# Kernel optimization log

Measured on AMD Instinct MI355X. Metric: run time of the kernel, lower is better.

Reference implementation:

```python
import jax, jax.numpy as jnp
import numpy as np
from jax import lax

MASK_STEEP = 4.0
MASK_SHIFT = 0.5
RESIST_TH = 0.225
RESIST_STEEP = 50.0
MAX_DOSE = 1.02
MIN_DOSE = 0.98
KD = 35  # kernel_dim1 == kernel_dim2


def setup_inputs() -> dict:
    key = jax.random.key(0)
    ks = jax.random.split(key, 7)
    N, H, W, K = 2, 1024, 1024, 24
    return {
        "mask_tile": jax.random.uniform(ks[0], (N, 1, H, W), dtype=jnp.float32),
        "kernel_focus_r": jax.random.normal(ks[1], (K, KD, KD), dtype=jnp.float32) * 0.02,
        "kernel_focus_i": jax.random.normal(ks[2], (K, KD, KD), dtype=jnp.float32) * 0.02,
        "kernel_defocus_r": jax.random.normal(ks[3], (K, KD, KD), dtype=jnp.float32) * 0.02,
        "kernel_defocus_i": jax.random.normal(ks[4], (K, KD, KD), dtype=jnp.float32) * 0.02,
        "kernel_focus_scale": jax.random.uniform(ks[5], (K, 1, 1), dtype=jnp.float32),
        "kernel_defocus_scale": jax.random.uniform(ks[6], (K, 1, 1), dtype=jnp.float32),
    }


def _avepool3(x):
    # nn.AvgPool2d(kernel=3, stride=1, pad=1) with count_include_pad=True ==
    # conv with a 3x3 ones/9 kernel and zero padding.
    k = jnp.ones((1, 1, 3, 3), x.dtype) / 9.0
    return lax.conv_general_dilated(
        x, k, window_strides=(1, 1), padding=[(1, 1), (1, 1)],
        dimension_numbers=("NCHW", "OIHW", "NCHW"))


def _dose_branch(spec, dose, kernel, scale, h, w):
    # spec: [N,1,KD,KD] complex; kernel: [K,KD,KD] complex; scale: [K,1,1]
    x = (spec * dose) * kernel[None]                 # [N,K,KD,KD] (repeat_interleave via broadcast, C=1)
    x = jnp.fft.ifft2(x, s=(h, w))                   # zero-pad to full tile, [N,K,h,w] complex
    inten = (x.real * x.real + x.imag * x.imag) * scale[None]
    inten = jnp.sum(inten, axis=1, keepdims=True)    # [N,1,h,w]
    resist = jax.nn.sigmoid(RESIST_STEEP * (inten - RESIST_TH))
    return resist, inten


def reference(mask_tile, kernel_focus_r, kernel_focus_i, kernel_defocus_r,
              kernel_defocus_i, kernel_focus_scale, kernel_defocus_scale):
    n, _, h, w = mask_tile.shape
    off = h // 2 - KD // 2
    mask = _avepool3(mask_tile)
    mask = jax.nn.sigmoid(MASK_STEEP * (mask - MASK_SHIFT))
    mf = jnp.fft.fftshift(jnp.fft.fft2(mask), axes=(-2, -1))  # [N,1,h,w] complex64
    spec = mf[:, :, off:off + KD, off:off + KD]               # [N,1,KD,KD]
    kf = kernel_focus_r + 1j * kernel_focus_i
    kdf = kernel_defocus_r + 1j * kernel_defocus_i
    nominal, x_out = _dose_branch(spec, 1.0, kf, kernel_focus_scale, h, w)
    outer, x_out_max = _dose_branch(spec, MAX_DOSE, kf, kernel_focus_scale, h, w)
    inner, x_out_min = _dose_branch(spec, MIN_DOSE, kdf, kernel_defocus_scale, h, w)
    return (nominal, inner, outer, x_out, x_out_min, x_out_max)
```

## Files before the change

kernel.cpp:

```cpp
#include <hip/hip_runtime.h>
#include <math.h>

#define NBATCH 2
#define HH 1024
#define WW 1024
#define KKER 24
#define KDIM 35
#define NPIX (HH*WW)
#define KSQ (KDIM*KDIM)
#define NDA 69
#define NTAU 9
#define NFR 18

#define G_OFF    0
#define SPEC_OFF (G_OFF + NBATCH*HH*NFR*2)
#define VP_OFF   (SPEC_OFF + NBATCH*KSQ*2)
#define V_OFF    (VP_OFF + NBATCH*2*KKER*NDA*KDIM*2)

__device__ __forceinline__ float2 cmadd(float2 p, float2 w, float2 u) {
    return make_float2(fmaf(p.x, w.x, fmaf(-p.y, w.y, u.x)),
                       fmaf(p.x, w.y, fmaf( p.y, w.x, u.y)));
}
__device__ __forceinline__ float sigm(float v) {
    return 1.f / (1.f + expf(-v));
}

__global__ __launch_bounds__(320) void fwd_rows(const float* __restrict__ mt, float* __restrict__ ws) {
    __shared__ __align__(16) float vs[1024];
    __shared__ float row[1056];
    __shared__ float2 twl[1024];
    __shared__ float2 P[16 * NFR];
    int bid = blockIdx.x;
    int n = bid >> 10, y = bid & 1023;
    int t = threadIdx.x;
    const float* base = mt + (size_t)n * NPIX;
    if (t < 256) {
        float4 a = ((const float4*)(base + (size_t)y * WW))[t];
        if (y > 0)    { float4 b = ((const float4*)(base + (size_t)(y - 1) * WW))[t];
                        a.x += b.x; a.y += b.y; a.z += b.z; a.w += b.w; }
        if (y < 1023) { float4 b = ((const float4*)(base + (size_t)(y + 1) * WW))[t];
                        a.x += b.x; a.y += b.y; a.z += b.z; a.w += b.w; }
        ((float4*)vs)[t] = a;
    }
    for (int j = t; j < 1024; j += 320) {
        float s, c;
        sincospif(-2.0f * (float)j * (1.0f / 1024.0f), &s, &c);
        twl[j] = make_float2(c, s);
    }
    __syncthreads();
    for (int x = t; x < 1024; x += 320) {
        float s = vs[x];
        if (x > 0)    s += vs[x - 1];
        if (x < 1023) s += vs[x + 1];
        s *= (1.0f / 9.0f);
        row[x + (x >> 5)] = sigm(4.0f * (s - 0.5f));
    }
    __syncthreads();
    if (t < 16 * NFR) {
        int q = t / NFR, m = t - q * NFR;
        float2 cm = twl[m];
        float ar = 0.f, ai = 0.f;
        #pragma unroll
        for (int sc = 0; sc < 2; ++sc) {
            int xs = q * 64 + sc * 32;
            unsigned j0 = ((unsigned)(m * xs)) & 1023u;
            float2 wv = twl[j0];
            float wr = wv.x, wi = wv.y;
            int rb = xs + (xs >> 5);
            #pragma unroll
            for (int i = 0; i < 32; ++i) {
                float val = row[rb + i];
                ar = fmaf(val, wr, ar);
                ai = fmaf(val, wi, ai);
                float nwr = fmaf(wr, cm.x, -wi * cm.y);
                float nwi = fmaf(wr, cm.y,  wi * cm.x);
                wr = nwr; wi = nwi;
            }
        }
        P[t] = make_float2(ar, ai);
    }
    __syncthreads();
    if (t < NFR) {
        float gr = 0.f, gi = 0.f;
        #pragma unroll
        for (int q = 0; q < 16; ++q) {
            gr += P[q * NFR + t].x;
            gi += P[q * NFR + t].y;
        }
        float2* Gp = (float2*)(ws + G_OFF) + (size_t)(n * HH + y) * NFR + t;
        *Gp = make_float2(gr, gi);
    }
}

__global__ __launch_bounds__(320) void fwd_cols(float* __restrict__ ws) {
    __shared__ float2 twl[1024];
    __shared__ float2 P[16 * NFR];
    int bid = blockIdx.x;
    int n = bid / KDIM, a = bid - n * KDIM;
    int t = threadIdx.x;
    for (int j = t; j < 1024; j += 320) {
        float s, c;
        sincospif(-2.0f * (float)j * (1.0f / 1024.0f), &s, &c);
        twl[j] = make_float2(c, s);
    }
    __syncthreads();
    if (t < 16 * NFR) {
        int g = t / NFR, mb = t - g * NFR;
        int ma = a - 17;
        int y0 = g * 64;
        const float2* Gp = (const float2*)(ws + G_OFF) + (size_t)n * HH * NFR + mb;
        float ar = 0.f, ai = 0.f;
        for (int i = 0; i < 64; ++i) {
            int y = y0 + i;
            unsigned j = ((unsigned)(ma * y)) & 1023u;
            float2 g2 = Gp[(size_t)y * NFR];
            float2 cc = twl[j];
            ar = fmaf(g2.x, cc.x, ar); ar = fmaf(-g2.y, cc.y, ar);
            ai = fmaf(g2.x, cc.y, ai); ai = fmaf( g2.y, cc.x, ai);
        }
        P[t] = make_float2(ar, ai);
    }
    __syncthreads();
    if (t < NFR) {
        float sr = 0.f, si = 0.f;
        #pragma unroll
        for (int g = 0; g < 16; ++g) { sr += P[g * NFR + t].x; si += P[g * NFR + t].y; }
        float2* Sp = (float2*)(ws + SPEC_OFF) + (size_t)n * KSQ;
        Sp[a * KDIM + (17 + t)] = make_float2(sr, si);
        if (t > 0)
            Sp[(34 - a) * KDIM + (17 - t)] = make_float2(sr, -si);
    }
}

#define VCOLS 43
__global__ __launch_bounds__(320) void mk_V(float* __restrict__ ws,
        const float* __restrict__ kfr, const float* __restrict__ kfi,
        const float* __restrict__ kdr, const float* __restrict__ kdi,
        const float* __restrict__ kfs, const float* __restrict__ kds) {
    __shared__ float2 Xp[KDIM * VCOLS];
    int bid = blockIdx.x;
    int tau = bid % NTAU; int r = bid / NTAU;
    int k = r % KKER; r /= KKER;
    int br = r & 1; int n = r >> 1;
    int t = threadIdx.x;
    for (int i = t; i < KDIM * VCOLS; i += 320) Xp[i] = make_float2(0.f, 0.f);
    __syncthreads();
    const float* kr = (br ? kdr : kfr) + (size_t)k * KSQ;
    const float* ki = (br ? kdi : kfi) + (size_t)k * KSQ;
    const float* sp = ws + SPEC_OFF + (size_t)n * KSQ * 2;
    for (int i = t; i < KSQ; i += 320) {
        int a = i / KDIM, b = i - a * KDIM;
        float srr = sp[2*i], sii = sp[2*i + 1];
        float krr = kr[i], kii = ki[i];
        Xp[a * VCOLS + b] = make_float2(srr * krr - sii * kii, srr * kii + sii * krr);
    }
    __syncthreads();
    const float INVN = 0x1p-40f;
    float s = (br ? kds[k] * (0.98f * 0.98f) : kfs[k]) * INVN;

    int dbg  = t >> 6;
    int lane = t & 63;
    int apSlot = lane & 7;
    int dai8   = lane >> 3;
    int dai = tau * 8 + dai8;
    int da  = dai - 34;
    int db0 = dbg * 8;
    int nbp = KDIM - db0;

    int daiHi = tau * 8 + 7; if (daiHi > NDA - 1) daiHi = NDA - 1;
    int daLo = tau * 8 - 34, daHi = daiHi - 34;
    int apLo = (-daHi > 0) ? -daHi : 0;
    int apHi = KDIM - daLo; if (apHi > KDIM) apHi = KDIM;

    float2 acc[8];
    #pragma unroll
    for (int j = 0; j < 8; ++j) acc[j] = make_float2(0.f, 0.f);

    for (int ap = apLo + apSlot; ap < apHi; ap += 8) {
        bool act = ((unsigned)(ap + da) < (unsigned)KDIM) && (dai < NDA);
        if (act) {
            const float2* rx = Xp + (ap + da) * VCOLS + db0;
            const float2* ry = Xp + ap * VCOLS;
            float2 w[8];
            #pragma unroll
            for (int j = 0; j < 8; ++j) w[j] = rx[j];
            int bp = 0;
            for (; bp + 8 <= nbp; bp += 8) {
                #pragma unroll
                for (int u = 0; u < 8; ++u) {
                    float2 yv = ry[bp + u];
                    #pragma unroll
                    for (int j = 0; j < 8; ++j) {
                        acc[j].x = fmaf(w[j].x, yv.x, acc[j].x);
                        acc[j].x = fmaf(w[j].y, yv.y, acc[j].x);
                        acc[j].y = fmaf(w[j].y, yv.x, acc[j].y);
                        acc[j].y = fmaf(-w[j].x, yv.y, acc[j].y);
                    }
                    #pragma unroll
                    for (int j = 0; j < 7; ++j) w[j] = w[j + 1];
                    w[7] = rx[bp + u + 8];
                }
            }
            for (; bp < nbp; ++bp) {
                float2 yv = ry[bp];
                #pragma unroll
                for (int j = 0; j < 8; ++j) {
                    acc[j].x = fmaf(w[j].x, yv.x, acc[j].x);
                    acc[j].x = fmaf(w[j].y, yv.y, acc[j].x);
                    acc[j].y = fmaf(w[j].y, yv.x, acc[j].y);
                    acc[j].y = fmaf(-w[j].x, yv.y, acc[j].y);
                }
                #pragma unroll
                for (int j = 0; j < 7; ++j) w[j] = w[j + 1];
                w[7] = rx[bp + 8];
            }
        }
    }
    #pragma unroll
    for (int j = 0; j < 8; ++j) {
        acc[j].x += __shfl_xor(acc[j].x, 1); acc[j].y += __shfl_xor(acc[j].y, 1);
        acc[j].x += __shfl_xor(acc[j].x, 2); acc[j].y += __shfl_xor(acc[j].y, 2);
        acc[j].x += __shfl_xor(acc[j].x, 4); acc[j].y += __shfl_xor(acc[j].y, 4);
    }
    if (apSlot == 0 && dai < NDA) {
        int nb = n * 2 + br;
        float2* vp = (float2*)(ws + VP_OFF);
        size_t vb = (((size_t)nb * KKER + k) * NDA + dai) * KDIM;
        #pragma unroll
        for (int j = 0; j < 8; ++j) {
            int db = db0 + j;
            if (db < KDIM)
                vp[vb + db] = make_float2(s * acc[j].x, s * acc[j].y);
        }
    }
}

__global__ __launch_bounds__(64) void reduce_V(float* __restrict__ ws) {
    int bid = blockIdx.x;
    int nb = bid / NDA, dai = bid - nb * NDA;
    int t = threadIdx.x;
    if (t < KDIM) {
        const float2* vp = (const float2*)(ws + VP_OFF);
        float sr = 0.f, si = 0.f;
        #pragma unroll
        for (int k = 0; k < KKER; ++k) {
            float2 v = vp[(((size_t)nb * KKER + k) * NDA + dai) * KDIM + t];
            sr += v.x; si += v.y;
        }
        ((float2*)(ws + V_OFF))[((size_t)nb * NDA + dai) * KDIM + t] = make_float2(sr, si);
    }
}

#define YPB 2
__global__ __launch_bounds__(256) void litho_fused(const float* __restrict__ ws,
                                                   float* __restrict__ out) {
    __shared__ float2 twl[1024];
    __shared__ float2 Vl[NDA * KDIM];
    __shared__ float2 Ul[YPB][KDIM];
    int bid = blockIdx.x;
    int yc = bid & 511; int nb = bid >> 9;
    int t = threadIdx.x;
    for (int j = t; j < 1024; j += 256) {
        float s, c;
        sincospif(-2.0f * (float)j * (1.0f / 1024.0f), &s, &c);
        twl[j] = make_float2(c, s);
    }
    const float2* Vg = (const float2*)(ws + V_OFF) + (size_t)nb * NDA * KDIM;
    for (int i = t; i < NDA * KDIM; i += 256) Vl[i] = Vg[i];
    __syncthreads();
    if (t < YPB * KDIM) {
        int yl = t / KDIM, db = t - yl * KDIM;
        int y = yc * YPB + yl;
        float ar = 0.f, ai = 0.f;
        for (int dai = 0; dai < NDA; ++dai) {
            unsigned j = ((unsigned)(y * (dai - 34))) & 1023u;
            float2 cc = twl[j];
            float cr = cc.x, ci = -cc.y;
            float2 v = Vl[dai * KDIM + db];
            ar = fmaf(v.x, cr, ar); ar = fmaf(-v.y, ci, ar);
            ai = fmaf(v.x, ci, ai); ai = fmaf( v.y, cr, ai);
        }
        Ul[yl][db] = make_float2(ar, ai);
    }
    __syncthreads();
    int n = nb >> 1, br = nb & 1;
    float2 z  = twl[t];              z.y  = -z.y;
    float2 z2 = twl[(2*t) & 1023];   z2.y = -z2.y;
    float2 z3 = twl[(3*t) & 1023];   z3.y = -z3.y;
    float2 w  = twl[(4*t) & 1023];   w.y  = -w.y;
    const size_t OS = (size_t)NBATCH * NPIX;
    #pragma unroll
    for (int yl = 0; yl < YPB; ++yl) {
        int y = yc * YPB + yl;
        float2 P0 = Ul[yl][32], P1 = Ul[yl][33], P2 = Ul[yl][34], P3 = make_float2(0.f, 0.f);
        #pragma unroll
        for (int q = 7; q >= 0; --q) {
            P0 = cmadd(P0, w, Ul[yl][4*q]);
            P1 = cmadd(P1, w, Ul[yl][4*q+1]);
            P2 = cmadd(P2, w, Ul[yl][4*q+2]);
            P3 = cmadd(P3, w, Ul[yl][4*q+3]);
        }
        float U0r = Ul[yl][0].x;
        float A1x = P1.x * z.x  - P1.y * z.y,  A1y = P1.x * z.y  + P1.y * z.x;
        float A2x = P2.x * z2.x - P2.y * z2.y;
        float A3x = P3.x * z3.x - P3.y * z3.y, A3y = P3.x * z3.y + P3.y * z3.x;
        float Re4[4];
        Re4[0] = P0.x + A1x + A2x + A3x;
        Re4[1] = P0.x - A1y - A2x + A3y;
        Re4[2] = P0.x - A1x + A2x - A3x;
        Re4[3] = P0.x + A1y - A2x - A3y;
        size_t obase = (size_t)n * NPIX + (size_t)y * WW;
        if (br == 0) {
            #pragma unroll
            for (int c = 0; c < 4; ++c) {
                int x = t + c * 256;
                float If   = fmaf(2.f, Re4[c], -U0r);
                float Imax = If * (1.02f * 1.02f);
                out[0 * OS + obase + x] = sigm(50.f * (If   - 0.225f));
                out[2 * OS + obase + x] = sigm(50.f * (Imax - 0.225f));
                out[3 * OS + obase + x] = If;
                out[5 * OS + obase + x] = Imax;
            }
        } else {
            #pragma unroll
            for (int c = 0; c < 4; ++c) {
                int x = t + c * 256;
                float Id = fmaf(2.f, Re4[c], -U0r);
                out[1 * OS + obase + x] = sigm(50.f * (Id - 0.225f));
                out[4 * OS + obase + x] = Id;
            }
        }
    }
}

extern "C" void kernel_launch(void* const* d_in, const int* in_sizes, int n_in,
                              void* d_out, int out_size, void* d_ws, size_t ws_size,
                              hipStream_t stream) {
    (void)in_sizes; (void)n_in; (void)out_size; (void)ws_size;
    const float* mt  = (const float*)d_in[0];
    const float* kfr = (const float*)d_in[1];
    const float* kfi = (const float*)d_in[2];
    const float* kdr = (const float*)d_in[3];
    const float* kdi = (const float*)d_in[4];
    const float* kfs = (const float*)d_in[5];
    const float* kds = (const float*)d_in[6];
    float* out = (float*)d_out;
    float* ws  = (float*)d_ws;

    hipLaunchKernelGGL(fwd_rows,    dim3(NBATCH * HH),              dim3(320), 0, stream, mt, ws);
    hipLaunchKernelGGL(fwd_cols,    dim3(NBATCH * KDIM),            dim3(320), 0, stream, ws);
    hipLaunchKernelGGL(mk_V,        dim3(NBATCH * 2 * KKER * NTAU), dim3(320), 0, stream,
                       ws, kfr, kfi, kdr, kdi, kfs, kds);
    hipLaunchKernelGGL(reduce_V,    dim3(NBATCH * 2 * NDA),         dim3(64),  0, stream, ws);
    hipLaunchKernelGGL(litho_fused, dim3(NBATCH * 2 * 512),         dim3(256), 0, stream, ws, out);
}
```

Before: 144.6 us.

## Fuse pipeline stages into one cooperative persistent kernel with grid syncs

Replaces the five separate launches with a single cooperative kernel of 512 persistent blocks that runs the row DFT, column DFT, V accumulation and output synthesis as phases separated by grid.sync. The per-kernel V partials and the reduce_V pass are replaced by atomicAdd into a V buffer that is zeroed during phase 1, and the spectrum is stored half-size and mirrored through Hermitian symmetry on read. The goal is to remove launch gaps and the extra reduction pass. In exchange it adds grid-wide barrier cost, lower parallelism in some phases (for example only 70 blocks active in phase 2), and float atomics whose summation order is nondeterministic. A non-cooperative four-launch fallback is kept in case the cooperative launch fails.

New measurement: 487.3 us. 237% more time.

```diff
diff --git a/kernel.cpp b/kernel.cpp
--- a/kernel.cpp
+++ b/kernel.cpp
@@ -1,5 +1,8 @@
 #include <hip/hip_runtime.h>
+#include <hip/hip_cooperative_groups.h>
 #include <math.h>
+
+namespace cg = cooperative_groups;
 
 #define NBATCH 2
 #define HH 1024
@@ -11,11 +14,14 @@
 #define NDA 69
 #define NTAU 9
 #define NFR 18
-
-#define G_OFF    0
-#define SPEC_OFF (G_OFF + NBATCH*HH*NFR*2)
-#define VP_OFF   (SPEC_OFF + NBATCH*KSQ*2)
-#define V_OFF    (VP_OFF + NBATCH*2*KKER*NDA*KDIM*2)
+#define VCOLS 43
+#define GRID 512
+#define TPB 256
+
+#define G_OFF 0
+#define S_OFF (G_OFF + NBATCH*HH*NFR*2)
+#define V_OFF (S_OFF + NBATCH*KDIM*NFR*2)
+#define V_FLOATS (NBATCH*2*NDA*KDIM*2)
 
 __device__ __forceinline__ float2 cmadd(float2 p, float2 w, float2 u) {
     return make_float2(fmaf(p.x, w.x, fmaf(-p.y, w.y, u.x)),
@@ -25,282 +31,252 @@
     return 1.f / (1.f + expf(-v));
 }
 
-__global__ __launch_bounds__(320) void fwd_rows(const float* __restrict__ mt, float* __restrict__ ws) {
-    __shared__ __align__(16) float vs[1024];
-    __shared__ float row[1056];
-    __shared__ float2 twl[1024];
-    __shared__ float2 P[16 * NFR];
-    int bid = blockIdx.x;
-    int n = bid >> 10, y = bid & 1023;
-    int t = threadIdx.x;
-    const float* base = mt + (size_t)n * NPIX;
-    if (t < 256) {
-        float4 a = ((const float4*)(base + (size_t)y * WW))[t];
-        if (y > 0)    { float4 b = ((const float4*)(base + (size_t)(y - 1) * WW))[t];
-                        a.x += b.x; a.y += b.y; a.z += b.z; a.w += b.w; }
-        if (y < 1023) { float4 b = ((const float4*)(base + (size_t)(y + 1) * WW))[t];
-                        a.x += b.x; a.y += b.y; a.z += b.z; a.w += b.w; }
-        ((float4*)vs)[t] = a;
-    }
-    for (int j = t; j < 1024; j += 320) {
+struct SMem {
+    union {
+        struct { float vs[1024]; float row[1024]; float2 P[256]; } p1;
+        struct { float2 Xp[KDIM * VCOLS]; } p3;
+        struct { float2 Vl[NDA * KDIM]; float2 Ul[8][KDIM]; } p4;
+    } u;
+    float2 twl[1024];
+};
+
+__device__ __forceinline__ void gen_twl(SMem& sm, int t) {
+    for (int j = t; j < 1024; j += TPB) {
         float s, c;
         sincospif(-2.0f * (float)j * (1.0f / 1024.0f), &s, &c);
-        twl[j] = make_float2(c, s);
-    }
+        sm.twl[j] = make_float2(c, s);
+    }
+}
+
+__device__ void phase1(SMem& sm, const float* __restrict__ mt, float* __restrict__ ws,
+                       int bid, int stride, int t) {
+    if (bid >= stride - 8) {
+        int sl = bid - (stride - 8);
+        const int chunk = V_FLOATS / 8;
+        for (int i = sl * chunk + t; i < (sl + 1) * chunk; i += TPB)
+            ws[V_OFF + i] = 0.f;
+    }
+    for (int r = bid; r < NBATCH * HH; r += stride) {
+        int n = r >> 10, y = r & 1023;
+        const float* base = mt + (size_t)n * NPIX;
+        __syncthreads();
+        {
+            float4 a = ((const float4*)(base + (size_t)y * WW))[t];
+            if (y > 0)    { float4 b = ((const float4*)(base + (size_t)(y - 1) * WW))[t];
+                            a.x += b.x; a.y += b.y; a.z += b.z; a.w += b.w; }
+            if (y < 1023) { float4 b = ((const float4*)(base + (size_t)(y + 1) * WW))[t];
+                            a.x += b.x; a.y += b.y; a.z += b.z; a.w += b.w; }
+            ((float4*)sm.u.p1.vs)[t] = a;
+        }
+        __syncthreads();
+        for (int x = t; x < 1024; x += TPB) {
+            float s = sm.u.p1.vs[x];
+            if (x > 0)    s += sm.u.p1.vs[x - 1];
+            if (x < 1023) s += sm.u.p1.vs[x + 1];
+            sm.u.p1.row[x] = sigm(4.0f * (s * (1.0f / 9.0f) - 0.5f));
+        }
+        __syncthreads();
+        if (t < 14 * NFR) {
+            int g = t / NFR, m = t - NFR * g;
+            int xs = (g << 10) / 14, xe = ((g + 1) << 10) / 14;
+            float2 cm = sm.twl[m];
+            float ar = 0.f, ai = 0.f;
+            for (int x0 = xs; x0 < xe; x0 += 32) {
+                float2 wv = sm.twl[((unsigned)(m * x0)) & 1023u];
+                float wr = wv.x, wi = wv.y;
+                int xl = (x0 + 32 < xe) ? x0 + 32 : xe;
+                for (int x = x0; x < xl; ++x) {
+                    float val = sm.u.p1.row[x];
+                    ar = fmaf(val, wr, ar);
+                    ai = fmaf(val, wi, ai);
+                    float nwr = fmaf(wr, cm.x, -wi * cm.y);
+                    float nwi = fmaf(wr, cm.y,  wi * cm.x);
+                    wr = nwr; wi = nwi;
+                }
+            }
+            sm.u.p1.P[t] = make_float2(ar, ai);
+        }
+        __syncthreads();
+        if (t < NFR) {
+            float gr = 0.f, gi = 0.f;
+            #pragma unroll
+            for (int g = 0; g < 14; ++g) {
+                gr += sm.u.p1.P[g * NFR + t].x;
+                gi += sm.u.p1.P[g * NFR + t].y;
+            }
+            float2* Gp = (float2*)(ws + G_OFF) + (size_t)(n * HH + y) * NFR + t;
+            *Gp = make_float2(gr, gi);
+        }
+    }
+}
+
+__device__ void phase2(SMem& sm, float* __restrict__ ws, int bid, int t) {
+    if (bid >= NBATCH * KDIM) return;
+    int n = bid / KDIM, a = bid - n * KDIM;
     __syncthreads();
-    for (int x = t; x < 1024; x += 320) {
-        float s = vs[x];
-        if (x > 0)    s += vs[x - 1];
-        if (x < 1023) s += vs[x + 1];
-        s *= (1.0f / 9.0f);
-        row[x + (x >> 5)] = sigm(4.0f * (s - 0.5f));
-    }
-    __syncthreads();
-    if (t < 16 * NFR) {
-        int q = t / NFR, m = t - q * NFR;
-        float2 cm = twl[m];
-        float ar = 0.f, ai = 0.f;
-        #pragma unroll
-        for (int sc = 0; sc < 2; ++sc) {
-            int xs = q * 64 + sc * 32;
-            unsigned j0 = ((unsigned)(m * xs)) & 1023u;
-            float2 wv = twl[j0];
-            float wr = wv.x, wi = wv.y;
-            int rb = xs + (xs >> 5);
-            #pragma unroll
-            for (int i = 0; i < 32; ++i) {
-                float val = row[rb + i];
-                ar = fmaf(val, wr, ar);
-                ai = fmaf(val, wi, ai);
-                float nwr = fmaf(wr, cm.x, -wi * cm.y);
-                float nwi = fmaf(wr, cm.y,  wi * cm.x);
-                wr = nwr; wi = nwi;
-            }
-        }
-        P[t] = make_float2(ar, ai);
-    }
-    __syncthreads();
-    if (t < NFR) {
-        float gr = 0.f, gi = 0.f;
-        #pragma unroll
-        for (int q = 0; q < 16; ++q) {
-            gr += P[q * NFR + t].x;
-            gi += P[q * NFR + t].y;
-        }
-        float2* Gp = (float2*)(ws + G_OFF) + (size_t)(n * HH + y) * NFR + t;
-        *Gp = make_float2(gr, gi);
-    }
-}
-
-__global__ __launch_bounds__(320) void fwd_cols(float* __restrict__ ws) {
-    __shared__ float2 twl[1024];
-    __shared__ float2 P[16 * NFR];
-    int bid = blockIdx.x;
-    int n = bid / KDIM, a = bid - n * KDIM;
-    int t = threadIdx.x;
-    for (int j = t; j < 1024; j += 320) {
-        float s, c;
-        sincospif(-2.0f * (float)j * (1.0f / 1024.0f), &s, &c);
-        twl[j] = make_float2(c, s);
-    }
-    __syncthreads();
-    if (t < 16 * NFR) {
-        int g = t / NFR, mb = t - g * NFR;
+    if (t < 14 * NFR) {
+        int g = t / NFR, mb = t - NFR * g;
+        int ys = (g << 10) / 14, ye = ((g + 1) << 10) / 14;
         int ma = a - 17;
-        int y0 = g * 64;
         const float2* Gp = (const float2*)(ws + G_OFF) + (size_t)n * HH * NFR + mb;
         float ar = 0.f, ai = 0.f;
-        for (int i = 0; i < 64; ++i) {
-            int y = y0 + i;
-            unsigned j = ((unsigned)(ma * y)) & 1023u;
+        for (int y = ys; y < ye; ++y) {
             float2 g2 = Gp[(size_t)y * NFR];
-            float2 cc = twl[j];
+            float2 cc = sm.twl[((unsigned)(ma * y)) & 1023u];
             ar = fmaf(g2.x, cc.x, ar); ar = fmaf(-g2.y, cc.y, ar);
             ai = fmaf(g2.x, cc.y, ai); ai = fmaf( g2.y, cc.x, ai);
         }
-        P[t] = make_float2(ar, ai);
+        sm.u.p1.P[t] = make_float2(ar, ai);
     }
     __syncthreads();
     if (t < NFR) {
         float sr = 0.f, si = 0.f;
         #pragma unroll
-        for (int g = 0; g < 16; ++g) { sr += P[g * NFR + t].x; si += P[g * NFR + t].y; }
-        float2* Sp = (float2*)(ws + SPEC_OFF) + (size_t)n * KSQ;
-        Sp[a * KDIM + (17 + t)] = make_float2(sr, si);
-        if (t > 0)
-            Sp[(34 - a) * KDIM + (17 - t)] = make_float2(sr, -si);
-    }
-}
-
-#define VCOLS 43
-__global__ __launch_bounds__(320) void mk_V(float* __restrict__ ws,
+        for (int g = 0; g < 14; ++g) { sr += sm.u.p1.P[g * NFR + t].x; si += sm.u.p1.P[g * NFR + t].y; }
+        ((float2*)(ws + S_OFF))[(size_t)(n * KDIM + a) * NFR + t] = make_float2(sr, si);
+    }
+}
+
+__device__ void phase3(SMem& sm, float* __restrict__ ws,
         const float* __restrict__ kfr, const float* __restrict__ kfi,
         const float* __restrict__ kdr, const float* __restrict__ kdi,
-        const float* __restrict__ kfs, const float* __restrict__ kds) {
-    __shared__ float2 Xp[KDIM * VCOLS];
-    int bid = blockIdx.x;
-    int tau = bid % NTAU; int r = bid / NTAU;
-    int k = r % KKER; r /= KKER;
-    int br = r & 1; int n = r >> 1;
-    int t = threadIdx.x;
-    for (int i = t; i < KDIM * VCOLS; i += 320) Xp[i] = make_float2(0.f, 0.f);
+        const float* __restrict__ kfs, const float* __restrict__ kds,
+        int bid, int stride, int t) {
+    for (int i = t; i < KDIM * 8; i += TPB) {
+        int a = i >> 3, c = KDIM + (i & 7);
+        sm.u.p3.Xp[a * VCOLS + c] = make_float2(0.f, 0.f);
+    }
+    for (int task = bid; task < 4 * KKER * NTAU; task += stride) {
+        int tau = task / 96; int rem = task - tau * 96;
+        int nb = rem / KKER; int k = rem - nb * KKER;
+        int br = nb & 1, n = nb >> 1;
+        __syncthreads();
+        const float* kr = (br ? kdr : kfr) + (size_t)k * KSQ;
+        const float* ki = (br ? kdi : kfi) + (size_t)k * KSQ;
+        const float2* Sp = (const float2*)(ws + S_OFF) + (size_t)n * KDIM * NFR;
+        for (int i = t; i < KSQ; i += TPB) {
+            int a = i / KDIM, b = i - a * KDIM;
+            float2 s2;
+            if (b >= 17) s2 = Sp[a * NFR + (b - 17)];
+            else { float2 q = Sp[(34 - a) * NFR + (17 - b)]; s2 = make_float2(q.x, -q.y); }
+            float krr = kr[i], kii = ki[i];
+            sm.u.p3.Xp[a * VCOLS + b] =
+                make_float2(s2.x * krr - s2.y * kii, s2.x * kii + s2.y * krr);
+        }
+        __syncthreads();
+        float s = (br ? kds[k] * (0.98f * 0.98f) : kfs[k]) * 0x1p-40f;
+        int wv = t >> 6, lane = t & 63;
+        int apSlot = lane & 7, dai8 = lane >> 3;
+        int dai = tau * 8 + dai8, da = dai - 34;
+        int daiHi = tau * 8 + 7; if (daiHi > NDA - 1) daiHi = NDA - 1;
+        int apLo = -(daiHi - 34); if (apLo < 0) apLo = 0;
+        int apHi = KDIM - (tau * 8 - 34); if (apHi > KDIM) apHi = KDIM;
+        int oct = (wv + task) & 3;
+        int npass = (oct == 3) ? 2 : 1;
+        bool lv = (dai < NDA);
+        for (int p = 0; p < npass; ++p) {
+            int db0 = p ? 32 : oct * 8;
+            int nbp = KDIM - db0;
+            float2 acc[8];
+            #pragma unroll
+            for (int j = 0; j < 8; ++j) acc[j] = make_float2(0.f, 0.f);
+            for (int ap = apLo + apSlot; ap < apHi; ap += 8) {
+                if (lv && ((unsigned)(ap + da) < (unsigned)KDIM)) {
+                    const float2* rx = sm.u.p3.Xp + (ap + da) * VCOLS + db0;
+                    const float2* ry = sm.u.p3.Xp + ap * VCOLS;
+                    float2 w[8];
+                    #pragma unroll
+                    for (int j = 0; j < 8; ++j) w[j] = rx[j];
+                    int bp = 0;
+                    for (; bp + 8 <= nbp; bp += 8) {
+                        #pragma unroll
+                        for (int u = 0; u < 8; ++u) {
+                            float2 yv = ry[bp + u];
+                            #pragma unroll
+                            for (int j = 0; j < 8; ++j) {
+                                acc[j].x = fmaf(w[j].x, yv.x, acc[j].x);
+                                acc[j].x = fmaf(w[j].y, yv.y, acc[j].x);
+                                acc[j].y = fmaf(w[j].y, yv.x, acc[j].y);
+                                acc[j].y = fmaf(-w[j].x, yv.y, acc[j].y);
+                            }
+                            #pragma unroll
+                            for (int j = 0; j < 7; ++j) w[j] = w[j + 1];
+                            w[7] = rx[bp + u + 8];
+                        }
+                    }
+                    for (; bp < nbp; ++bp) {
+                        float2 yv = ry[bp];
+                        #pragma unroll
+                        for (int j = 0; j < 8; ++j) {
+                            acc[j].x = fmaf(w[j].x, yv.x, acc[j].x);
+                            acc[j].x = fmaf(w[j].y, yv.y, acc[j].x);
+                            acc[j].y = fmaf(w[j].y, yv.x, acc[j].y);
+                            acc[j].y = fmaf(-w[j].x, yv.y, acc[j].y);
+                        }
+                        #pragma unroll
+                        for (int j = 0; j < 7; ++j) w[j] = w[j + 1];
+                        w[7] = rx[bp + 8];
+                    }
+                }
+            }
+            #pragma unroll
+            for (int j = 0; j < 8; ++j) {
+                acc[j].x += __shfl_xor(acc[j].x, 1); acc[j].y += __shfl_xor(acc[j].y, 1);
+                acc[j].x += __shfl_xor(acc[j].x, 2); acc[j].y += __shfl_xor(acc[j].y, 2);
+                acc[j].x += __shfl_xor(acc[j].x, 4); acc[j].y += __shfl_xor(acc[j].y, 4);
+            }
+            if (apSlot == 0 && lv) {
+                float* vb = ws + V_OFF + (((size_t)nb * NDA + dai) * KDIM + db0) * 2;
+                #pragma unroll
+                for (int j = 0; j < 8; ++j) if (db0 + j < KDIM) {
+                    atomicAdd(vb + 2 * j,     s * acc[j].x);
+                    atomicAdd(vb + 2 * j + 1, s * acc[j].y);
+                }
+            }
+        }
+    }
+}
+
+__device__ void phase4(SMem& sm, const float* __restrict__ ws, float* __restrict__ out,
+                       int bid, int t) {
+    int nb = bid >> 7, yc = bid & 127;
+    int y0 = yc * 8;
+    const float2* Vg = (const float2*)(ws + V_OFF) + (size_t)nb * NDA * KDIM;
+    for (int i = t; i < NDA * KDIM; i += TPB) sm.u.p4.Vl[i] = Vg[i];
     __syncthreads();
-    const float* kr = (br ? kdr : kfr) + (size_t)k * KSQ;
-    const float* ki = (br ? kdi : kfi) + (size_t)k * KSQ;
-    const float* sp = ws + SPEC_OFF + (size_t)n * KSQ * 2;
-    for (int i = t; i < KSQ; i += 320) {
-        int a = i / KDIM, b = i - a * KDIM;
-        float srr = sp[2*i], sii = sp[2*i + 1];
-        float krr = kr[i], kii = ki[i];
-        Xp[a * VCOLS + b] = make_float2(srr * krr - sii * kii, srr * kii + sii * krr);
-    }
-    __syncthreads();
-    const float INVN = 0x1p-40f;
-    float s = (br ? kds[k] * (0.98f * 0.98f) : kfs[k]) * INVN;
-
-    int dbg  = t >> 6;
-    int lane = t & 63;
-    int apSlot = lane & 7;
-    int dai8   = lane >> 3;
-    int dai = tau * 8 + dai8;
-    int da  = dai - 34;
-    int db0 = dbg * 8;
-    int nbp = KDIM - db0;
-
-    int daiHi = tau * 8 + 7; if (daiHi > NDA - 1) daiHi = NDA - 1;
-    int daLo = tau * 8 - 34, daHi = daiHi - 34;
-    int apLo = (-daHi > 0) ? -daHi : 0;
-    int apHi = KDIM - daLo; if (apHi > KDIM) apHi = KDIM;
-
-    float2 acc[8];
-    #pragma unroll
-    for (int j = 0; j < 8; ++j) acc[j] = make_float2(0.f, 0.f);
-
-    for (int ap = apLo + apSlot; ap < apHi; ap += 8) {
-        bool act = ((unsigned)(ap + da) < (unsigned)KDIM) && (dai < NDA);
-        if (act) {
-            const float2* rx = Xp + (ap + da) * VCOLS + db0;
-            const float2* ry = Xp + ap * VCOLS;
-            float2 w[8];
-            #pragma unroll
-            for (int j = 0; j < 8; ++j) w[j] = rx[j];
-            int bp = 0;
-            for (; bp + 8 <= nbp; bp += 8) {
-                #pragma unroll
-                for (int u = 0; u < 8; ++u) {
-                    float2 yv = ry[bp + u];
-                    #pragma unroll
-                    for (int j = 0; j < 8; ++j) {
-                        acc[j].x = fmaf(w[j].x, yv.x, acc[j].x);
-                        acc[j].x = fmaf(w[j].y, yv.y, acc[j].x);
-                        acc[j].y = fmaf(w[j].y, yv.x, acc[j].y);
-                        acc[j].y = fmaf(-w[j].x, yv.y, acc[j].y);
-                    }
-                    #pragma unroll
-                    for (int j = 0; j < 7; ++j) w[j] = w[j + 1];
-                    w[7] = rx[bp + u + 8];
-                }
-            }
-            for (; bp < nbp; ++bp) {
-                float2 yv = ry[bp];
-                #pragma unroll
-                for (int j = 0; j < 8; ++j) {
-                    acc[j].x = fmaf(w[j].x, yv.x, acc[j].x);
-                    acc[j].x = fmaf(w[j].y, yv.y, acc[j].x);
-                    acc[j].y = fmaf(w[j].y, yv.x, acc[j].y);
-                    acc[j].y = fmaf(-w[j].x, yv.y, acc[j].y);
-                }
-                #pragma unroll
-                for (int j = 0; j < 7; ++j) w[j] = w[j + 1];
-                w[7] = rx[bp + 8];
-            }
-        }
-    }
-    #pragma unroll
-    for (int j = 0; j < 8; ++j) {
-        acc[j].x += __shfl_xor(acc[j].x, 1); acc[j].y += __shfl_xor(acc[j].y, 1);
-        acc[j].x += __shfl_xor(acc[j].x, 2); acc[j].y += __shfl_xor(acc[j].y, 2);
-        acc[j].x += __shfl_xor(acc[j].x, 4); acc[j].y += __shfl_xor(acc[j].y, 4);
-    }
-    if (apSlot == 0 && dai < NDA) {
-        int nb = n * 2 + br;
-        float2* vp = (float2*)(ws + VP_OFF);
-        size_t vb = (((size_t)nb * KKER + k) * NDA + dai) * KDIM;
-        #pragma unroll
-        for (int j = 0; j < 8; ++j) {
-            int db = db0 + j;
-            if (db < KDIM)
-                vp[vb + db] = make_float2(s * acc[j].x, s * acc[j].y);
-        }
-    }
-}
-
-__global__ __launch_bounds__(64) void reduce_V(float* __restrict__ ws) {
-    int bid = blockIdx.x;
-    int nb = bid / NDA, dai = bid - nb * NDA;
-    int t = threadIdx.x;
-    if (t < KDIM) {
-        const float2* vp = (const float2*)(ws + VP_OFF);
-        float sr = 0.f, si = 0.f;
-        #pragma unroll
-        for (int k = 0; k < KKER; ++k) {
-            float2 v = vp[(((size_t)nb * KKER + k) * NDA + dai) * KDIM + t];
-            sr += v.x; si += v.y;
-        }
-        ((float2*)(ws + V_OFF))[((size_t)nb * NDA + dai) * KDIM + t] = make_float2(sr, si);
-    }
-}
-
-#define YPB 2
-__global__ __launch_bounds__(256) void litho_fused(const float* __restrict__ ws,
-                                                   float* __restrict__ out) {
-    __shared__ float2 twl[1024];
-    __shared__ float2 Vl[NDA * KDIM];
-    __shared__ float2 Ul[YPB][KDIM];
-    int bid = blockIdx.x;
-    int yc = bid & 511; int nb = bid >> 9;
-    int t = threadIdx.x;
-    for (int j = t; j < 1024; j += 256) {
-        float s, c;
-        sincospif(-2.0f * (float)j * (1.0f / 1024.0f), &s, &c);
-        twl[j] = make_float2(c, s);
-    }
-    const float2* Vg = (const float2*)(ws + V_OFF) + (size_t)nb * NDA * KDIM;
-    for (int i = t; i < NDA * KDIM; i += 256) Vl[i] = Vg[i];
-    __syncthreads();
-    if (t < YPB * KDIM) {
-        int yl = t / KDIM, db = t - yl * KDIM;
-        int y = yc * YPB + yl;
+    for (int task = t; task < 8 * KDIM; task += TPB) {
+        int yl = task / KDIM, db = task - KDIM * yl;
+        int y = y0 + yl;
         float ar = 0.f, ai = 0.f;
         for (int dai = 0; dai < NDA; ++dai) {
-            unsigned j = ((unsigned)(y * (dai - 34))) & 1023u;
-            float2 cc = twl[j];
+            float2 cc = sm.twl[((unsigned)(y * (dai - 34))) & 1023u];
             float cr = cc.x, ci = -cc.y;
-            float2 v = Vl[dai * KDIM + db];
+            float2 v = sm.u.p4.Vl[dai * KDIM + db];
             ar = fmaf(v.x, cr, ar); ar = fmaf(-v.y, ci, ar);
             ai = fmaf(v.x, ci, ai); ai = fmaf( v.y, cr, ai);
         }
-        Ul[yl][db] = make_float2(ar, ai);
+        sm.u.p4.Ul[yl][db] = make_float2(ar, ai);
     }
     __syncthreads();
     int n = nb >> 1, br = nb & 1;
-    float2 z  = twl[t];              z.y  = -z.y;
-    float2 z2 = twl[(2*t) & 1023];   z2.y = -z2.y;
-    float2 z3 = twl[(3*t) & 1023];   z3.y = -z3.y;
-    float2 w  = twl[(4*t) & 1023];   w.y  = -w.y;
+    float2 z  = sm.twl[t];              z.y  = -z.y;
+    float2 z2 = sm.twl[(2 * t) & 1023]; z2.y = -z2.y;
+    float2 z3 = sm.twl[(3 * t) & 1023]; z3.y = -z3.y;
+    float2 w  = sm.twl[(4 * t) & 1023]; w.y  = -w.y;
     const size_t OS = (size_t)NBATCH * NPIX;
     #pragma unroll
-    for (int yl = 0; yl < YPB; ++yl) {
-        int y = yc * YPB + yl;
-        float2 P0 = Ul[yl][32], P1 = Ul[yl][33], P2 = Ul[yl][34], P3 = make_float2(0.f, 0.f);
+    for (int yl = 0; yl < 8; ++yl) {
+        int y = y0 + yl;
+        float2 P0 = sm.u.p4.Ul[yl][32], P1 = sm.u.p4.Ul[yl][33];
+        float2 P2 = sm.u.p4.Ul[yl][34], P3 = make_float2(0.f, 0.f);
         #pragma unroll
         for (int q = 7; q >= 0; --q) {
-            P0 = cmadd(P0, w, Ul[yl][4*q]);
-            P1 = cmadd(P1, w, Ul[yl][4*q+1]);
-            P2 = cmadd(P2, w, Ul[yl][4*q+2]);
-            P3 = cmadd(P3, w, Ul[yl][4*q+3]);
-        }
-        float U0r = Ul[yl][0].x;
+            P0 = cmadd(P0, w, sm.u.p4.Ul[yl][4 * q]);
+            P1 = cmadd(P1, w, sm.u.p4.Ul[yl][4 * q + 1]);
+            P2 = cmadd(P2, w, sm.u.p4.Ul[yl][4 * q + 2]);
+            P3 = cmadd(P3, w, sm.u.p4.Ul[yl][4 * q + 3]);
+        }
+        float U0r = sm.u.p4.Ul[yl][0].x;
         float A1x = P1.x * z.x  - P1.y * z.y,  A1y = P1.x * z.y  + P1.y * z.x;
         float A2x = P2.x * z2.x - P2.y * z2.y;
         float A3x = P3.x * z3.x - P3.y * z3.y, A3y = P3.x * z3.y + P3.y * z3.x;
@@ -331,6 +307,48 @@
             }
         }
     }
+}
+
+__global__ __launch_bounds__(TPB, 2) void mega(const float* __restrict__ mt,
+    const float* __restrict__ kfr, const float* __restrict__ kfi,
+    const float* __restrict__ kdr, const float* __restrict__ kdi,
+    const float* __restrict__ kfs, const float* __restrict__ kds,
+    float* __restrict__ out, float* __restrict__ ws)
+{
+    __shared__ SMem sm;
+    cg::grid_group grid = cg::this_grid();
+    int bid = blockIdx.x, t = threadIdx.x;
+    gen_twl(sm, t);
+    phase1(sm, mt, ws, bid, GRID, t);
+    __threadfence(); grid.sync();
+    phase2(sm, ws, bid, t);
+    __threadfence(); grid.sync();
+    phase3(sm, ws, kfr, kfi, kdr, kdi, kfs, kds, bid, GRID, t);
+    __threadfence(); grid.sync();
+    phase4(sm, ws, out, bid, t);
+}
+
+__global__ __launch_bounds__(TPB, 2) void k_p1(const float* __restrict__ mt, float* __restrict__ ws) {
+    __shared__ SMem sm;
+    gen_twl(sm, threadIdx.x);
+    phase1(sm, mt, ws, blockIdx.x, gridDim.x, threadIdx.x);
+}
+__global__ __launch_bounds__(TPB, 2) void k_p2(float* __restrict__ ws) {
+    __shared__ SMem sm;
+    gen_twl(sm, threadIdx.x);
+    phase2(sm, ws, blockIdx.x, threadIdx.x);
+}
+__global__ __launch_bounds__(TPB, 2) void k_p3(float* __restrict__ ws,
+        const float* __restrict__ kfr, const float* __restrict__ kfi,
+        const float* __restrict__ kdr, const float* __restrict__ kdi,
+        const float* __restrict__ kfs, const float* __restrict__ kds) {
+    __shared__ SMem sm;
+    phase3(sm, ws, kfr, kfi, kdr, kdi, kfs, kds, blockIdx.x, gridDim.x, threadIdx.x);
+}
+__global__ __launch_bounds__(TPB, 2) void k_p4(const float* __restrict__ ws, float* __restrict__ out) {
+    __shared__ SMem sm;
+    gen_twl(sm, threadIdx.x);
+    phase4(sm, ws, out, blockIdx.x, threadIdx.x);
 }
 
 extern "C" void kernel_launch(void* const* d_in, const int* in_sizes, int n_in,
@@ -347,10 +365,16 @@
     float* out = (float*)d_out;
     float* ws  = (float*)d_ws;
 
-    hipLaunchKernelGGL(fwd_rows,    dim3(NBATCH * HH),              dim3(320), 0, stream, mt, ws);
-    hipLaunchKernelGGL(fwd_cols,    dim3(NBATCH * KDIM),            dim3(320), 0, stream, ws);
-    hipLaunchKernelGGL(mk_V,        dim3(NBATCH * 2 * KKER * NTAU), dim3(320), 0, stream,
-                       ws, kfr, kfi, kdr, kdi, kfs, kds);
-    hipLaunchKernelGGL(reduce_V,    dim3(NBATCH * 2 * NDA),         dim3(64),  0, stream, ws);
-    hipLaunchKernelGGL(litho_fused, dim3(NBATCH * 2 * 512),         dim3(256), 0, stream, ws, out);
-}
+    void* kargs[] = { (void*)&mt, (void*)&kfr, (void*)&kfi, (void*)&kdr, (void*)&kdi,
+                      (void*)&kfs, (void*)&kds, (void*)&out, (void*)&ws };
+    hipError_t err = hipLaunchCooperativeKernel((void*)mega, dim3(GRID), dim3(TPB),
+                                                kargs, 0, stream);
+    if (err != hipSuccess) {
+        (void)hipGetLastError();
+        hipLaunchKernelGGL(k_p1, dim3(GRID),          dim3(TPB), 0, stream, mt, ws);
+        hipLaunchKernelGGL(k_p2, dim3(NBATCH * KDIM), dim3(TPB), 0, stream, ws);
+        hipLaunchKernelGGL(k_p3, dim3(GRID),          dim3(TPB), 0, stream,
+                           ws, kfr, kfi, kdr, kdi, kfs, kds);
+        hipLaunchKernelGGL(k_p4, dim3(GRID),          dim3(TPB), 0, stream, ws, out);
+    }
+}
```

## Replace V partial-sum reduction with atomics and rebalance mk_V and fwd_cols work

Applied to the files above, without the earlier changes.

Removes the reduce_V kernel and the per-kernel partial buffer. mk_V now atomically adds each kernel's scaled contribution into V, and V is zeroed by two extra blocks appended to the fwd_cols launch. mk_V goes from 5 to 8 waves, splitting the triangular db work across waves with load-balancing tables, and fwd_cols uses 1024 threads with 56 row groups instead of 16. This drops one launch and a global round-trip, but it adds float atomics (non-deterministic summation order) and depends on the zeroing blocks finishing before mk_V runs.

Result: slower. 202.3 us (+39.8%).

```diff
diff --git a/kernel.cpp b/kernel.cpp
--- a/kernel.cpp
+++ b/kernel.cpp
@@ -11,11 +11,12 @@
 #define NDA 69
 #define NTAU 9
 #define NFR 18
-
-#define G_OFF    0
-#define SPEC_OFF (G_OFF + NBATCH*HH*NFR*2)
-#define VP_OFF   (SPEC_OFF + NBATCH*KSQ*2)
-#define V_OFF    (VP_OFF + NBATCH*2*KKER*NDA*KDIM*2)
+#define VCOLS 43
+
+#define G_OFF 0
+#define S_OFF (G_OFF + NBATCH*HH*NFR*2)
+#define V_OFF (S_OFF + NBATCH*KSQ*2)
+#define V_FLOATS (NBATCH*2*NDA*KDIM*2)
 
 __device__ __forceinline__ float2 cmadd(float2 p, float2 w, float2 u) {
     return make_float2(fmaf(p.x, w.x, fmaf(-p.y, w.y, u.x)),
@@ -92,29 +93,33 @@
     }
 }
 
-__global__ __launch_bounds__(320) void fwd_cols(float* __restrict__ ws) {
+__global__ __launch_bounds__(1024) void fwd_cols(float* __restrict__ ws) {
     __shared__ float2 twl[1024];
-    __shared__ float2 P[16 * NFR];
+    __shared__ float2 P[56 * NFR];
     int bid = blockIdx.x;
+    int t = threadIdx.x;
+    if (bid >= NBATCH * KDIM) {
+        int half = bid - NBATCH * KDIM;
+        for (int i = half * (V_FLOATS / 2) + t; i < (half + 1) * (V_FLOATS / 2); i += 1024)
+            ws[V_OFF + i] = 0.f;
+        return;
+    }
     int n = bid / KDIM, a = bid - n * KDIM;
-    int t = threadIdx.x;
-    for (int j = t; j < 1024; j += 320) {
+    {
         float s, c;
-        sincospif(-2.0f * (float)j * (1.0f / 1024.0f), &s, &c);
-        twl[j] = make_float2(c, s);
-    }
-    __syncthreads();
-    if (t < 16 * NFR) {
-        int g = t / NFR, mb = t - g * NFR;
+        sincospif(-2.0f * (float)t * (1.0f / 1024.0f), &s, &c);
+        twl[t] = make_float2(c, s);
+    }
+    __syncthreads();
+    if (t < 56 * NFR) {
+        int g = t / NFR, mb = t - NFR * g;
+        int ys = (g << 10) / 56, ye = ((g + 1) << 10) / 56;
         int ma = a - 17;
-        int y0 = g * 64;
         const float2* Gp = (const float2*)(ws + G_OFF) + (size_t)n * HH * NFR + mb;
         float ar = 0.f, ai = 0.f;
-        for (int i = 0; i < 64; ++i) {
-            int y = y0 + i;
-            unsigned j = ((unsigned)(ma * y)) & 1023u;
+        for (int y = ys; y < ye; ++y) {
             float2 g2 = Gp[(size_t)y * NFR];
-            float2 cc = twl[j];
+            float2 cc = twl[((unsigned)(ma * y)) & 1023u];
             ar = fmaf(g2.x, cc.x, ar); ar = fmaf(-g2.y, cc.y, ar);
             ai = fmaf(g2.x, cc.y, ai); ai = fmaf( g2.y, cc.x, ai);
         }
@@ -124,16 +129,15 @@
     if (t < NFR) {
         float sr = 0.f, si = 0.f;
         #pragma unroll
-        for (int g = 0; g < 16; ++g) { sr += P[g * NFR + t].x; si += P[g * NFR + t].y; }
-        float2* Sp = (float2*)(ws + SPEC_OFF) + (size_t)n * KSQ;
+        for (int g = 0; g < 56; ++g) { sr += P[g * NFR + t].x; si += P[g * NFR + t].y; }
+        float2* Sp = (float2*)(ws + S_OFF) + (size_t)n * KSQ;
         Sp[a * KDIM + (17 + t)] = make_float2(sr, si);
         if (t > 0)
             Sp[(34 - a) * KDIM + (17 - t)] = make_float2(sr, -si);
     }
 }
 
-#define VCOLS 43
-__global__ __launch_bounds__(320) void mk_V(float* __restrict__ ws,
+__global__ __launch_bounds__(512) void mk_V(float* __restrict__ ws,
         const float* __restrict__ kfr, const float* __restrict__ kfi,
         const float* __restrict__ kdr, const float* __restrict__ kdi,
         const float* __restrict__ kfs, const float* __restrict__ kds) {
@@ -143,52 +147,65 @@
     int k = r % KKER; r /= KKER;
     int br = r & 1; int n = r >> 1;
     int t = threadIdx.x;
-    for (int i = t; i < KDIM * VCOLS; i += 320) Xp[i] = make_float2(0.f, 0.f);
+    for (int i = t; i < KDIM * VCOLS; i += 512) Xp[i] = make_float2(0.f, 0.f);
     __syncthreads();
     const float* kr = (br ? kdr : kfr) + (size_t)k * KSQ;
     const float* ki = (br ? kdi : kfi) + (size_t)k * KSQ;
-    const float* sp = ws + SPEC_OFF + (size_t)n * KSQ * 2;
-    for (int i = t; i < KSQ; i += 320) {
+    const float* sp = ws + S_OFF + (size_t)n * KSQ * 2;
+    for (int i = t; i < KSQ; i += 512) {
         int a = i / KDIM, b = i - a * KDIM;
         float srr = sp[2*i], sii = sp[2*i + 1];
         float krr = kr[i], kii = ki[i];
         Xp[a * VCOLS + b] = make_float2(srr * krr - sii * kii, srr * kii + sii * krr);
     }
     __syncthreads();
-    const float INVN = 0x1p-40f;
-    float s = (br ? kds[k] * (0.98f * 0.98f) : kfs[k]) * INVN;
-
-    int dbg  = t >> 6;
-    int lane = t & 63;
-    int apSlot = lane & 7;
-    int dai8   = lane >> 3;
-    int dai = tau * 8 + dai8;
-    int da  = dai - 34;
-    int db0 = dbg * 8;
-    int nbp = KDIM - db0;
-
+    float s = (br ? kds[k] * (0.98f * 0.98f) : kfs[k]) * 0x1p-40f;
+
+    int wv = t >> 6, lane = t & 63;
+    int apSlot = lane & 7, dai8 = lane >> 3;
+    int dai = tau * 8 + dai8, da = dai - 34;
     int daiHi = tau * 8 + 7; if (daiHi > NDA - 1) daiHi = NDA - 1;
-    int daLo = tau * 8 - 34, daHi = daiHi - 34;
-    int apLo = (-daHi > 0) ? -daHi : 0;
-    int apHi = KDIM - daLo; if (apHi > KDIM) apHi = KDIM;
-
-    float2 acc[8];
-    #pragma unroll
-    for (int j = 0; j < 8; ++j) acc[j] = make_float2(0.f, 0.f);
-
-    for (int ap = apLo + apSlot; ap < apHi; ap += 8) {
-        bool act = ((unsigned)(ap + da) < (unsigned)KDIM) && (dai < NDA);
-        if (act) {
-            const float2* rx = Xp + (ap + da) * VCOLS + db0;
-            const float2* ry = Xp + ap * VCOLS;
-            float2 w[8];
-            #pragma unroll
-            for (int j = 0; j < 8; ++j) w[j] = rx[j];
-            int bp = 0;
-            for (; bp + 8 <= nbp; bp += 8) {
+    int apLo = -(daiHi - 34); if (apLo < 0) apLo = 0;
+    int apHi = KDIM - (tau * 8 - 34); if (apHi > KDIM) apHi = KDIM;
+    bool lv = (dai < NDA);
+
+    const int octTab[8] = {0, 0, 0, 1, 1, 2, 2, 3};
+    const int b0Tab[8]  = {0, 12, 24, 0, 13, 0, 9, 0};
+    const int b1Tab[8]  = {12, 24, 35, 13, 27, 9, 19, 11};
+    int npass = (wv == 7) ? 2 : 1;
+    for (int p = 0; p < npass; ++p) {
+        int db0 = p ? 32 : octTab[wv] * 8;
+        int b0  = p ? 0  : b0Tab[wv];
+        int b1  = p ? 3  : b1Tab[wv];
+        float2 acc[8];
+        #pragma unroll
+        for (int j = 0; j < 8; ++j) acc[j] = make_float2(0.f, 0.f);
+        for (int ap = apLo + apSlot; ap < apHi; ap += 8) {
+            if (lv && ((unsigned)(ap + da) < (unsigned)KDIM)) {
+                const float2* rx = Xp + (ap + da) * VCOLS + db0;
+                const float2* ry = Xp + ap * VCOLS;
+                float2 w[8];
                 #pragma unroll
-                for (int u = 0; u < 8; ++u) {
-                    float2 yv = ry[bp + u];
+                for (int j = 0; j < 8; ++j) w[j] = rx[b0 + j];
+                int bp = b0;
+                for (; bp + 8 <= b1; bp += 8) {
+                    #pragma unroll
+                    for (int u = 0; u < 8; ++u) {
+                        float2 yv = ry[bp + u];
+                        #pragma unroll
+                        for (int j = 0; j < 8; ++j) {
+                            acc[j].x = fmaf(w[j].x, yv.x, acc[j].x);
+                            acc[j].x = fmaf(w[j].y, yv.y, acc[j].x);
+                            acc[j].y = fmaf(w[j].y, yv.x, acc[j].y);
+                            acc[j].y = fmaf(-w[j].x, yv.y, acc[j].y);
+                        }
+                        #pragma unroll
+                        for (int j = 0; j < 7; ++j) w[j] = w[j + 1];
+                        w[7] = rx[bp + u + 8];
+                    }
+                }
+                for (; bp < b1; ++bp) {
+                    float2 yv = ry[bp];
                     #pragma unroll
                     for (int j = 0; j < 8; ++j) {
                         acc[j].x = fmaf(w[j].x, yv.x, acc[j].x);
@@ -198,56 +215,25 @@
                     }
                     #pragma unroll
                     for (int j = 0; j < 7; ++j) w[j] = w[j + 1];
-                    w[7] = rx[bp + u + 8];
+                    w[7] = rx[bp + 8];
                 }
             }
-            for (; bp < nbp; ++bp) {
-                float2 yv = ry[bp];
-                #pragma unroll
-                for (int j = 0; j < 8; ++j) {
-                    acc[j].x = fmaf(w[j].x, yv.x, acc[j].x);
-                    acc[j].x = fmaf(w[j].y, yv.y, acc[j].x);
-                    acc[j].y = fmaf(w[j].y, yv.x, acc[j].y);
-                    acc[j].y = fmaf(-w[j].x, yv.y, acc[j].y);
-                }
-                #pragma unroll
-                for (int j = 0; j < 7; ++j) w[j] = w[j + 1];
-                w[7] = rx[bp + 8];
-            }
-        }
-    }
-    #pragma unroll
-    for (int j = 0; j < 8; ++j) {
-        acc[j].x += __shfl_xor(acc[j].x, 1); acc[j].y += __shfl_xor(acc[j].y, 1);
-        acc[j].x += __shfl_xor(acc[j].x, 2); acc[j].y += __shfl_xor(acc[j].y, 2);
-        acc[j].x += __shfl_xor(acc[j].x, 4); acc[j].y += __shfl_xor(acc[j].y, 4);
-    }
-    if (apSlot == 0 && dai < NDA) {
-        int nb = n * 2 + br;
-        float2* vp = (float2*)(ws + VP_OFF);
-        size_t vb = (((size_t)nb * KKER + k) * NDA + dai) * KDIM;
+        }
         #pragma unroll
         for (int j = 0; j < 8; ++j) {
-            int db = db0 + j;
-            if (db < KDIM)
-                vp[vb + db] = make_float2(s * acc[j].x, s * acc[j].y);
-        }
-    }
-}
-
-__global__ __launch_bounds__(64) void reduce_V(float* __restrict__ ws) {
-    int bid = blockIdx.x;
-    int nb = bid / NDA, dai = bid - nb * NDA;
-    int t = threadIdx.x;
-    if (t < KDIM) {
-        const float2* vp = (const float2*)(ws + VP_OFF);
-        float sr = 0.f, si = 0.f;
-        #pragma unroll
-        for (int k = 0; k < KKER; ++k) {
-            float2 v = vp[(((size_t)nb * KKER + k) * NDA + dai) * KDIM + t];
-            sr += v.x; si += v.y;
-        }
-        ((float2*)(ws + V_OFF))[((size_t)nb * NDA + dai) * KDIM + t] = make_float2(sr, si);
+            acc[j].x += __shfl_xor(acc[j].x, 1); acc[j].y += __shfl_xor(acc[j].y, 1);
+            acc[j].x += __shfl_xor(acc[j].x, 2); acc[j].y += __shfl_xor(acc[j].y, 2);
+            acc[j].x += __shfl_xor(acc[j].x, 4); acc[j].y += __shfl_xor(acc[j].y, 4);
+        }
+        if (apSlot == 0 && lv) {
+            int nb = n * 2 + br;
+            float* vb = ws + V_OFF + (((size_t)nb * NDA + dai) * KDIM + db0) * 2;
+            #pragma unroll
+            for (int j = 0; j < 8; ++j) if (db0 + j < KDIM) {
+                atomicAdd(vb + 2 * j,     s * acc[j].x);
+                atomicAdd(vb + 2 * j + 1, s * acc[j].y);
+            }
+        }
     }
 }
 
@@ -273,8 +259,7 @@
         int y = yc * YPB + yl;
         float ar = 0.f, ai = 0.f;
         for (int dai = 0; dai < NDA; ++dai) {
-            unsigned j = ((unsigned)(y * (dai - 34))) & 1023u;
-            float2 cc = twl[j];
+            float2 cc = twl[((unsigned)(y * (dai - 34))) & 1023u];
             float cr = cc.x, ci = -cc.y;
             float2 v = Vl[dai * KDIM + db];
             ar = fmaf(v.x, cr, ar); ar = fmaf(-v.y, ci, ar);
@@ -347,10 +332,9 @@
     float* out = (float*)d_out;
     float* ws  = (float*)d_ws;
 
-    hipLaunchKernelGGL(fwd_rows,    dim3(NBATCH * HH),              dim3(320), 0, stream, mt, ws);
-    hipLaunchKernelGGL(fwd_cols,    dim3(NBATCH * KDIM),            dim3(320), 0, stream, ws);
-    hipLaunchKernelGGL(mk_V,        dim3(NBATCH * 2 * KKER * NTAU), dim3(320), 0, stream,
+    hipLaunchKernelGGL(fwd_rows,    dim3(NBATCH * HH),              dim3(320),  0, stream, mt, ws);
+    hipLaunchKernelGGL(fwd_cols,    dim3(NBATCH * KDIM + 2),        dim3(1024), 0, stream, ws);
+    hipLaunchKernelGGL(mk_V,        dim3(NBATCH * 2 * KKER * NTAU), dim3(512),  0, stream,
                        ws, kfr, kfi, kdr, kdi, kfs, kds);
-    hipLaunchKernelGGL(reduce_V,    dim3(NBATCH * 2 * NDA),         dim3(64),  0, stream, ws);
-    hipLaunchKernelGGL(litho_fused, dim3(NBATCH * 2 * 512),         dim3(256), 0, stream, ws, out);
-}
+    hipLaunchKernelGGL(litho_fused, dim3(NBATCH * 2 * 512),         dim3(256),  0, stream, ws, out);
+}
```
